# Performance work log

Measured on AMD Instinct MI355X. Metric: run time of the kernel, lower is better.

## Reference

```python
import jax, jax.numpy as jnp
import numpy as np

N_NODES, N_EDGES, MAX_NB = 40000, 80000, 4
INPUT_SIZE, NODE_FDIM, HIDDEN = 384, 256, 256
DEPTH = 6


def setup_inputs() -> dict:
    key = jax.random.key(0)
    ks = jax.random.split(key, 16)
    s = 0.05  # weight init scale
    return {
        "fnode": jax.random.normal(ks[0], (N_NODES, NODE_FDIM), dtype=jnp.float32),
        "fmess": jax.random.normal(ks[1], (N_EDGES, INPUT_SIZE), dtype=jnp.float32),
        "agraph": jax.random.randint(ks[2], (N_NODES, MAX_NB), 0, N_EDGES),
        "bgraph": jax.random.randint(ks[3], (N_EDGES, MAX_NB), 0, N_EDGES),
        "mask": jnp.ones((N_NODES, 1), dtype=jnp.float32),
        "Wz": jax.random.normal(ks[4], (INPUT_SIZE + HIDDEN, HIDDEN), dtype=jnp.float32) * s,
        "bz": jnp.zeros((HIDDEN,), dtype=jnp.float32),
        "Wr": jax.random.normal(ks[5], (INPUT_SIZE, HIDDEN), dtype=jnp.float32) * s,
        "Ur": jax.random.normal(ks[6], (HIDDEN, HIDDEN), dtype=jnp.float32) * s,
        "bur": jnp.zeros((HIDDEN,), dtype=jnp.float32),
        "Wh": jax.random.normal(ks[7], (INPUT_SIZE + HIDDEN, HIDDEN), dtype=jnp.float32) * s,
        "bh": jnp.zeros((HIDDEN,), dtype=jnp.float32),
        "Wo": jax.random.normal(ks[8], (NODE_FDIM + HIDDEN, HIDDEN), dtype=jnp.float32) * s,
        "bo": jnp.zeros((HIDDEN,), dtype=jnp.float32),
        "depth": DEPTH,
    }


def reference(fnode, fmess, agraph, bgraph, mask, Wz, bz, Wr, Ur, bur, Wh, bh, Wo, bo, depth):
    E, H = fmess.shape[0], Wz.shape[1]
    # message 0 is padding -> kept at zero each step (mask[0,0]=0 in torch GRU)
    msg_mask = jnp.ones((E, 1), dtype=fmess.dtype).at[0, 0].set(0.0)
    rx = fmess @ Wr  # precomputable: [E, H], reset gate input term

    def step(h, _):
        h_nei = h[bgraph]                      # [E, nb, H] gather
        sum_h = h_nei.sum(axis=1)              # [E, H]
        z = jax.nn.sigmoid(jnp.concatenate([fmess, sum_h], axis=1) @ Wz + bz)
        r = jax.nn.sigmoid(rx[:, None, :] + h_nei @ Ur + bur)  # [E, nb, H]
        sum_gh = (r * h_nei).sum(axis=1)
        pre_h = jnp.tanh(jnp.concatenate([fmess, sum_gh], axis=1) @ Wh + bh)
        h_new = ((1.0 - z) * sum_h + z * pre_h) * msg_mask
        return h_new, None

    h0 = jnp.zeros((E, H), dtype=fmess.dtype)
    h, _ = jax.lax.scan(step, h0, None, length=depth)

    nei_message = h[agraph].sum(axis=1)        # [N, H] gather-sum over incoming edges
    node_hiddens = jax.nn.relu(jnp.concatenate([fnode, nei_message], axis=1) @ Wo + bo)
    return node_hiddens * mask, h
```

## Files before the change

kernel.cpp:

```cpp
#include <hip/hip_runtime.h>
#include <stdint.h>

#define N_NODES 40000
#define N_EDGES 80000
#define HID 256
#define DEPTH_FIXED 6
#define NPAD 40064
#define MT 32

typedef __bf16 bf16;
typedef __bf16 bf16x4 __attribute__((ext_vector_type(4)));
typedef __bf16 bf16x8 __attribute__((ext_vector_type(8)));
typedef float f32x4 __attribute__((ext_vector_type(4)));

#define TPAD 136
#define APAD 264

__device__ __forceinline__ float sigmoidf_(float x) { return 1.f / (1.f + __expf(-x)); }
__device__ __forceinline__ float tanhf_(float x) { float e = __expf(2.f * x); return 1.f - 2.f / (e + 1.f); }

__device__ __forceinline__ void gld_lds16(const void* g, void* l) {
    __builtin_amdgcn_global_load_lds(
        (const __attribute__((address_space(1))) uint32_t*)g,
        (__attribute__((address_space(3))) uint32_t*)l, 16, 0, 0);
}

__device__ __forceinline__ void stage_tile(const bf16* __restrict__ src, int ld, int r0, int k0,
                                           bf16* lds, int tid) {
#pragma unroll
    for (int jj = 0; jj < 2; ++jj) {
        int s = jj * 256 + tid;
        int c = s ^ ((s >> 3) & 3);
        gld_lds16(src + (size_t)(r0 + (c >> 2)) * ld + k0 + (c & 3) * 8, lds + s * 8);
    }
}

__device__ __forceinline__ void mfma_tile(const bf16* lds_a, const bf16* lds_b,
                                          int wm, int wn, int lane, f32x4 (&acc)[4][4]) {
    const int li = lane & 15, quad = lane >> 4;
    const int sw = quad ^ ((li >> 1) & 3);
    bf16x8 a[4], b[4];
#pragma unroll
    for (int i = 0; i < 4; ++i)
        a[i] = *(const bf16x8*)(lds_a + ((wm * 64 + i * 16 + li) * 4 + sw) * 8);
#pragma unroll
    for (int j = 0; j < 4; ++j)
        b[j] = *(const bf16x8*)(lds_b + ((wn * 64 + j * 16 + li) * 4 + sw) * 8);
#pragma unroll
    for (int i = 0; i < 4; ++i)
#pragma unroll
        for (int j = 0; j < 4; ++j)
            acc[i][j] = __builtin_amdgcn_mfma_f32_16x16x32_bf16(a[i], b[j], acc[i][j], 0, 0, 0);
}

__global__ __launch_bounds__(256, 3) void step_fused_k(
    const int* __restrict__ bgraph, const bf16* __restrict__ Hcur,
    const bf16* __restrict__ HU, const bf16* __restrict__ P,
    const bf16* __restrict__ B1T, const bf16* __restrict__ B2T,
    bf16* __restrict__ Hnew, float* __restrict__ HF) {
    __shared__ __align__(16) bf16 sA1[MT * APAD];
    __shared__ __align__(16) bf16 sA2[MT * APAD];
    __shared__ __align__(16) bf16 sBst[256 * 32];
    const int tid = threadIdx.x, lane = tid & 63, wave = tid >> 6;
    const int m0 = blockIdx.x * MT;

    {
        const int r = tid >> 3, qc = tid & 7;
        const int e = m0 + r;
        const int4 nb = *(const int4*)(bgraph + (size_t)e * 4);
        const int bi[4] = {nb.x, nb.y, nb.z, nb.w};
        const bf16* prx = P + (size_t)e * 768 + qc * 32;
        bf16x8 rx[4];
#pragma unroll
        for (int c = 0; c < 4; ++c) rx[c] = *(const bf16x8*)(prx + c * 8);
        float sh[4][8] = {}, gh[4][8] = {};
#pragma unroll
        for (int j = 0; j < 4; ++j) {
            const bf16* hp = Hcur + (size_t)bi[j] * HID + qc * 32;
            const bf16* up = HU + (size_t)bi[j] * HID + qc * 32;
            bf16x8 hv[4], uv[4];
#pragma unroll
            for (int c = 0; c < 4; ++c) { hv[c] = *(const bf16x8*)(hp + c * 8); uv[c] = *(const bf16x8*)(up + c * 8); }
#pragma unroll
            for (int c = 0; c < 4; ++c)
#pragma unroll
                for (int u = 0; u < 8; ++u) {
                    float hf = (float)hv[c][u];
                    float rr = sigmoidf_((float)rx[c][u] + (float)uv[c][u]);
                    sh[c][u] += hf;
                    gh[c][u] += rr * hf;
                }
        }
#pragma unroll
        for (int c = 0; c < 4; ++c) {
            bf16x8 os, og;
#pragma unroll
            for (int u = 0; u < 8; ++u) { os[u] = (bf16)sh[c][u]; og[u] = (bf16)gh[c][u]; }
            *(bf16x8*)(sA1 + r * APAD + qc * 32 + c * 8) = os;
            *(bf16x8*)(sA2 + r * APAD + qc * 32 + c * 8) = og;
        }
    }
    __syncthreads();

    const int li = lane & 15, quad = lane >> 4;
    const int sw = quad ^ ((li >> 1) & 3);
    f32x4 accZ[2][4] = {}, accH[2][4] = {};
#pragma unroll
    for (int pass = 0; pass < 2; ++pass) {
        const bf16* BT = pass ? B2T : B1T;
        const bf16* sA = pass ? sA2 : sA1;
        for (int t = 0; t < 8; ++t) {
#pragma unroll
            for (int jj = 0; jj < 4; ++jj) {
                int s = jj * 256 + tid;
                int c = s ^ ((s >> 3) & 3);
                gld_lds16(BT + (size_t)(c >> 2) * 256 + t * 32 + (c & 3) * 8, sBst + s * 8);
            }
            __syncthreads();
            bf16x8 a[2], b[4];
#pragma unroll
            for (int i = 0; i < 2; ++i)
                a[i] = *(const bf16x8*)(sA + (i * 16 + li) * APAD + t * 32 + quad * 8);
#pragma unroll
            for (int j = 0; j < 4; ++j)
                b[j] = *(const bf16x8*)(sBst + ((wave * 64 + j * 16 + li) * 4 + sw) * 8);
#pragma unroll
            for (int i = 0; i < 2; ++i)
#pragma unroll
                for (int j = 0; j < 4; ++j) {
                    if (pass == 0) accZ[i][j] = __builtin_amdgcn_mfma_f32_16x16x32_bf16(a[i], b[j], accZ[i][j], 0, 0, 0);
                    else           accH[i][j] = __builtin_amdgcn_mfma_f32_16x16x32_bf16(a[i], b[j], accH[i][j], 0, 0, 0);
                }
            __syncthreads();
        }
    }

    bf16* tZ = sA2;
    bf16* tH = sBst;
#pragma unroll
    for (int i = 0; i < 2; ++i)
#pragma unroll
        for (int j = 0; j < 4; ++j) {
            const int col = wave * 64 + j * 16 + li;
#pragma unroll
            for (int r = 0; r < 4; ++r) {
                const int row = i * 16 + quad * 4 + r;
                tZ[row * APAD + col] = (bf16)accZ[i][j][r];
                tH[row * 256 + col] = (bf16)accH[i][j][r];
            }
        }
    __syncthreads();
#pragma unroll
    for (int s = 0; s < 4; ++s) {
        int v = s * 256 + tid;
        int lr = v >> 5, c8 = (v & 31) * 8;
        int e = m0 + lr;
        bf16x8 zl = *(const bf16x8*)(tZ + lr * APAD + c8);
        bf16x8 hl = *(const bf16x8*)(tH + lr * 256 + c8);
        bf16x8 shv = *(const bf16x8*)(sA1 + lr * APAD + c8);
        bf16x8 zx = *(const bf16x8*)(P + (size_t)e * 768 + 256 + c8);
        bf16x8 hx = *(const bf16x8*)(P + (size_t)e * 768 + 512 + c8);
        bf16x8 o;
        float of[8];
#pragma unroll
        for (int u = 0; u < 8; ++u) {
            float z = sigmoidf_((float)zl[u] + (float)zx[u]);
            float p = tanhf_((float)hl[u] + (float)hx[u]);
            float hn = (1.f - z) * (float)shv[u] + z * p;
            if (e == 0) hn = 0.f;
            o[u] = (bf16)hn;
            of[u] = hn;
        }
        *(bf16x8*)(Hnew + (size_t)e * HID + c8) = o;
        if (HF) {
            *(float4*)(HF + (size_t)e * HID + c8) = make_float4(of[0], of[1], of[2], of[3]);
            *(float4*)(HF + (size_t)e * HID + c8 + 4) = make_float4(of[4], of[5], of[6], of[7]);
        }
    }
}

__global__ __launch_bounds__(256) void gemm_single_k(
    const bf16* __restrict__ A, const bf16* __restrict__ BT,
    const float* __restrict__ bias, bf16* __restrict__ C, int K, int ldc) {
    __shared__ __align__(16) char smem[34816];
    bf16* sA = (bf16*)smem;
    bf16* sB = sA + 4096;
    const int tid = threadIdx.x, lane = tid & 63, wave = tid >> 6;
    const int wm = wave >> 1, wn = wave & 1;
    const int m0 = blockIdx.x * 128, n0 = blockIdx.y * 128;
    f32x4 acc[4][4] = {};
    for (int k0 = 0; k0 < K; k0 += 32) {
        stage_tile(A, K, m0, k0, sA, tid);
        stage_tile(BT, K, n0, k0, sB, tid);
        __syncthreads();
        mfma_tile(sA, sB, wm, wn, lane, acc);
        __syncthreads();
    }
    bf16* tC = (bf16*)smem;
#pragma unroll
    for (int i = 0; i < 4; ++i)
#pragma unroll
        for (int j = 0; j < 4; ++j) {
            const int col = wn * 64 + j * 16 + (lane & 15);
#pragma unroll
            for (int r = 0; r < 4; ++r) {
                const int lr = wm * 64 + i * 16 + (lane >> 4) * 4 + r;
                tC[lr * TPAD + col] = (bf16)acc[i][j][r];
            }
        }
    __syncthreads();
#pragma unroll
    for (int s = 0; s < 8; ++s) {
        int v = s * 256 + tid;
        int lr = v >> 4, c8 = (v & 15) * 8;
        bf16x8 cv = *(const bf16x8*)(tC + lr * TPAD + c8);
        bf16x8 o;
        if (bias) {
            float4 b0 = *(const float4*)(bias + n0 + c8);
            float4 b1 = *(const float4*)(bias + n0 + c8 + 4);
            o[0] = (bf16)((float)cv[0] + b0.x); o[1] = (bf16)((float)cv[1] + b0.y);
            o[2] = (bf16)((float)cv[2] + b0.z); o[3] = (bf16)((float)cv[3] + b0.w);
            o[4] = (bf16)((float)cv[4] + b1.x); o[5] = (bf16)((float)cv[5] + b1.y);
            o[6] = (bf16)((float)cv[6] + b1.z); o[7] = (bf16)((float)cv[7] + b1.w);
        } else {
            o = cv;
        }
        *(bf16x8*)(C + (size_t)(m0 + lr) * ldc + n0 + c8) = o;
    }
}

__global__ __launch_bounds__(256) void gemm_out_k(
    const bf16* __restrict__ A1, const bf16* __restrict__ A2,
    const bf16* __restrict__ B1T, const bf16* __restrict__ B2T,
    const float* __restrict__ bo, const float* __restrict__ mask, float* __restrict__ out) {
    __shared__ __align__(16) char smem[34816];
    bf16* s0 = (bf16*)smem;
    bf16* s1 = s0 + 4096;
    bf16* s2 = s1 + 4096;
    bf16* s3 = s2 + 4096;
    const int tid = threadIdx.x, lane = tid & 63, wave = tid >> 6;
    const int wm = wave >> 1, wn = wave & 1;
    const int m0 = blockIdx.x * 128, n0 = blockIdx.y * 128;
    f32x4 acc1[4][4] = {}, acc2[4][4] = {};
    for (int k0 = 0; k0 < 256; k0 += 32) {
        stage_tile(A1, 256, m0, k0, s0, tid);
        stage_tile(B1T, 256, n0, k0, s1, tid);
        stage_tile(A2, 256, m0, k0, s2, tid);
        stage_tile(B2T, 256, n0, k0, s3, tid);
        __syncthreads();
        mfma_tile(s0, s1, wm, wn, lane, acc1);
        mfma_tile(s2, s3, wm, wn, lane, acc2);
        __syncthreads();
    }
    bf16* tC = (bf16*)smem;
#pragma unroll
    for (int i = 0; i < 4; ++i)
#pragma unroll
        for (int j = 0; j < 4; ++j) {
            const int col = wn * 64 + j * 16 + (lane & 15);
#pragma unroll
            for (int r = 0; r < 4; ++r) {
                const int lr = wm * 64 + i * 16 + (lane >> 4) * 4 + r;
                tC[lr * TPAD + col] = (bf16)(acc1[i][j][r] + acc2[i][j][r]);
            }
        }
    __syncthreads();
#pragma unroll
    for (int s = 0; s < 8; ++s) {
        int v = s * 256 + tid;
        int lr = v >> 4, c8 = (v & 15) * 8;
        int grow = m0 + lr;
        if (grow >= N_NODES) continue;
        int gcol = n0 + c8;
        bf16x8 cv = *(const bf16x8*)(tC + lr * TPAD + c8);
        float4 b0 = *(const float4*)(bo + gcol);
        float4 b1 = *(const float4*)(bo + gcol + 4);
        float mk = mask[grow];
        float4 o0, o1;
        o0.x = fmaxf((float)cv[0] + b0.x, 0.f) * mk;
        o0.y = fmaxf((float)cv[1] + b0.y, 0.f) * mk;
        o0.z = fmaxf((float)cv[2] + b0.z, 0.f) * mk;
        o0.w = fmaxf((float)cv[3] + b0.w, 0.f) * mk;
        o1.x = fmaxf((float)cv[4] + b1.x, 0.f) * mk;
        o1.y = fmaxf((float)cv[5] + b1.y, 0.f) * mk;
        o1.z = fmaxf((float)cv[6] + b1.z, 0.f) * mk;
        o1.w = fmaxf((float)cv[7] + b1.w, 0.f) * mk;
        *(float4*)(out + (size_t)grow * 256 + gcol) = o0;
        *(float4*)(out + (size_t)grow * 256 + gcol + 4) = o1;
    }
}

__global__ __launch_bounds__(256) void gather_nei_k(
    const int* __restrict__ agraph, const bf16* __restrict__ H, bf16* __restrict__ nei) {
    int i = blockIdx.x * 256 + threadIdx.x;
    int v = i >> 5, c8 = (i & 31) * 8;
    bf16x8 o;
    if (v < N_NODES) {
        int4 nb = *(const int4*)(agraph + (size_t)v * 4);
        int bi[4] = {nb.x, nb.y, nb.z, nb.w};
        float s[8] = {};
#pragma unroll
        for (int j = 0; j < 4; ++j) {
            bf16x8 hv = *(const bf16x8*)(H + (size_t)bi[j] * HID + c8);
#pragma unroll
            for (int r = 0; r < 8; ++r) s[r] += (float)hv[r];
        }
#pragma unroll
        for (int r = 0; r < 8; ++r) o[r] = (bf16)s[r];
    } else {
#pragma unroll
        for (int r = 0; r < 8; ++r) o[r] = (bf16)0.f;
    }
    *(bf16x8*)(nei + (size_t)v * HID + c8) = o;
}

__global__ __launch_bounds__(256) void step1_k(const bf16* __restrict__ P, bf16* __restrict__ H) {
    int i = blockIdx.x * 256 + threadIdx.x;
    int e = i >> 5, c8 = (i & 31) * 8;
    bf16x8 zx = *(const bf16x8*)(P + (size_t)e * 768 + 256 + c8);
    bf16x8 hx = *(const bf16x8*)(P + (size_t)e * 768 + 512 + c8);
    bf16x8 o;
#pragma unroll
    for (int r = 0; r < 8; ++r) {
        float h = sigmoidf_((float)zx[r]) * tanhf_((float)hx[r]);
        if (e == 0) h = 0.f;
        o[r] = (bf16)h;
    }
    *(bf16x8*)(H + (size_t)e * HID + c8) = o;
}

__global__ void cvt_bf16_k(const float* __restrict__ src, bf16* __restrict__ dst, int n4) {
    int i = blockIdx.x * 256 + threadIdx.x;
    if (i >= n4) return;
    float4 v = ((const float4*)src)[i];
    bf16x4 o = {(bf16)v.x, (bf16)v.y, (bf16)v.z, (bf16)v.w};
    *((bf16x4*)dst + i) = o;
}

__global__ void cvt_fnode_k(const float* __restrict__ src, bf16* __restrict__ dst) {
    int i = blockIdx.x * 256 + threadIdx.x;
    int row = i >> 6;
    bf16x4 o = {(bf16)0.f, (bf16)0.f, (bf16)0.f, (bf16)0.f};
    if (row < N_NODES) {
        float4 v = ((const float4*)src)[i];
        o[0] = (bf16)v.x; o[1] = (bf16)v.y; o[2] = (bf16)v.z; o[3] = (bf16)v.w;
    }
    *((bf16x4*)dst + i) = o;
}

__global__ void prep_wpre_k(const float* __restrict__ Wr, const float* __restrict__ Wz,
                            const float* __restrict__ Wh, bf16* __restrict__ WT) {
    int idx = blockIdx.x * 256 + threadIdx.x;
    if (idx >= 768 * 384) return;
    int n = idx / 384, k = idx % 384;
    float v;
    if (n < 256) v = Wr[(size_t)k * 256 + n];
    else if (n < 512) v = Wz[(size_t)k * 256 + (n - 256)];
    else v = Wh[(size_t)k * 256 + (n - 512)];
    WT[idx] = (bf16)v;
}

__global__ void prep_bias_k(const float* __restrict__ bur, const float* __restrict__ bz,
                            const float* __restrict__ bh, float* __restrict__ bp) {
    int n = blockIdx.x * 256 + threadIdx.x;
    if (n >= 768) return;
    bp[n] = n < 256 ? bur[n] : (n < 512 ? bz[n - 256] : bh[n - 512]);
}

__global__ void prep_t256_k(const float* __restrict__ W, bf16* __restrict__ T, int roff) {
    int idx = blockIdx.x * 256 + threadIdx.x;
    int n = idx >> 8, k = idx & 255;
    T[idx] = (bf16)W[(size_t)(roff + k) * 256 + n];
}

extern "C" void kernel_launch(void* const* d_in, const int* in_sizes, int n_in,
                              void* d_out, int out_size, void* d_ws, size_t ws_size,
                              hipStream_t stream) {
    (void)in_sizes; (void)n_in; (void)out_size; (void)ws_size;
    const float* fnode = (const float*)d_in[0];
    const float* fmess = (const float*)d_in[1];
    const int* agraph = (const int*)d_in[2];
    const int* bgraph = (const int*)d_in[3];
    const float* mask = (const float*)d_in[4];
    const float* Wz = (const float*)d_in[5];
    const float* bz = (const float*)d_in[6];
    const float* Wr = (const float*)d_in[7];
    const float* Ur = (const float*)d_in[8];
    const float* bur = (const float*)d_in[9];
    const float* Wh = (const float*)d_in[10];
    const float* bh = (const float*)d_in[11];
    const float* Wo = (const float*)d_in[12];
    const float* bo = (const float*)d_in[13];
    float* out_node = (float*)d_out;
    float* out_h = out_node + (size_t)N_NODES * HID;

    char* ws = (char*)d_ws;
    size_t off = 0;
    auto alloc = [&](size_t b) -> char* { char* p = ws + off; off += (b + 255) & ~(size_t)255; return p; };
    bf16* P     = (bf16*)alloc((size_t)N_EDGES * 768 * 2);
    bf16* Hb0   = (bf16*)alloc((size_t)N_EDGES * HID * 2);
    bf16* Hb1   = (bf16*)alloc((size_t)N_EDGES * HID * 2);
    bf16* HU    = (bf16*)alloc((size_t)N_EDGES * HID * 2);
    bf16* fnodeB= (bf16*)alloc((size_t)NPAD * HID * 2);
    bf16* nei   = (bf16*)alloc((size_t)NPAD * HID * 2);
    bf16* WTpre = (bf16*)alloc((size_t)768 * 384 * 2);
    bf16* UrT   = (bf16*)alloc(65536 * 2);
    bf16* WzBT  = (bf16*)alloc(65536 * 2);
    bf16* WhBT  = (bf16*)alloc(65536 * 2);
    bf16* WoTT  = (bf16*)alloc(65536 * 2);
    bf16* WoBT  = (bf16*)alloc(65536 * 2);
    float* biasP= (float*)alloc(768 * 4);
    bf16* fmessB = Hb1;

    cvt_bf16_k<<<30000, 256, 0, stream>>>(fmess, fmessB, N_EDGES * 384 / 4);
    cvt_fnode_k<<<NPAD * 64 / 256, 256, 0, stream>>>(fnode, fnodeB);
    prep_wpre_k<<<(768 * 384 + 255) / 256, 256, 0, stream>>>(Wr, Wz, Wh, WTpre);
    prep_bias_k<<<3, 256, 0, stream>>>(bur, bz, bh, biasP);
    prep_t256_k<<<256, 256, 0, stream>>>(Ur, UrT, 0);
    prep_t256_k<<<256, 256, 0, stream>>>(Wz, WzBT, 384);
    prep_t256_k<<<256, 256, 0, stream>>>(Wh, WhBT, 384);
    prep_t256_k<<<256, 256, 0, stream>>>(Wo, WoTT, 0);
    prep_t256_k<<<256, 256, 0, stream>>>(Wo, WoBT, 256);

    gemm_single_k<<<dim3(625, 6), 256, 0, stream>>>(fmessB, WTpre, biasP, P, 384, 768);

    step1_k<<<N_EDGES * 32 / 256, 256, 0, stream>>>(P, Hb0);

    bf16* cur = Hb0;
    bf16* nxt = Hb1;
    for (int d = 2; d <= DEPTH_FIXED; ++d) {
        gemm_single_k<<<dim3(625, 2), 256, 0, stream>>>(cur, UrT, nullptr, HU, 256, 256);
        step_fused_k<<<N_EDGES / MT, 256, 0, stream>>>(bgraph, cur, HU, P, WzBT, WhBT, nxt,
                                                       d == DEPTH_FIXED ? out_h : nullptr);
        bf16* t = cur; cur = nxt; nxt = t;
    }

    gather_nei_k<<<NPAD * 32 / 256, 256, 0, stream>>>(agraph, cur, nei);
    gemm_out_k<<<dim3(313, 2), 256, 0, stream>>>(fnodeB, nei, WoTT, WoBT, bo, mask, out_node);
}
```

Measured before the change: 1.395 ms.

## Interleave H and H·Ur rows, read weights directly from global, drop staging LDS

H and its Ur projection now share one interleaved buffer with a 512-element row stride, so each neighbor gather reads a single contiguous 1 KB row instead of two separate rows. The fused step kernel no longer stages weight tiles into shared memory. Each wave loads its B fragments straight from global or L2, which removes per-tile barriers and the sBst buffer. The epilogue is split into two column halves so the transpose scratch fits in sA2, and the occupancy hint rises from 3 to 4 blocks. The risk is extra global and L2 traffic for the weights, since every block now rereads them without LDS reuse across waves.

```diff
diff --git a/kernel.cpp b/kernel.cpp
--- a/kernel.cpp
+++ b/kernel.cpp
@@ -15,6 +15,7 @@
 
 #define TPAD 136
 #define APAD 264
+#define TP2  132
 
 __device__ __forceinline__ float sigmoidf_(float x) { return 1.f / (1.f + __expf(-x)); }
 __device__ __forceinline__ float tanhf_(float x) { float e = __expf(2.f * x); return 1.f - 2.f / (e + 1.f); }
@@ -53,16 +54,16 @@
             acc[i][j] = __builtin_amdgcn_mfma_f32_16x16x32_bf16(a[i], b[j], acc[i][j], 0, 0, 0);
 }
 
-__global__ __launch_bounds__(256, 3) void step_fused_k(
-    const int* __restrict__ bgraph, const bf16* __restrict__ Hcur,
-    const bf16* __restrict__ HU, const bf16* __restrict__ P,
+__global__ __launch_bounds__(256, 4) void step_fused_k(
+    const int* __restrict__ bgraph, const bf16* __restrict__ HH,
+    const bf16* __restrict__ P,
     const bf16* __restrict__ B1T, const bf16* __restrict__ B2T,
-    bf16* __restrict__ Hnew, float* __restrict__ HF) {
+    bf16* __restrict__ HHn, float* __restrict__ HF) {
     __shared__ __align__(16) bf16 sA1[MT * APAD];
     __shared__ __align__(16) bf16 sA2[MT * APAD];
-    __shared__ __align__(16) bf16 sBst[256 * 32];
     const int tid = threadIdx.x, lane = tid & 63, wave = tid >> 6;
     const int m0 = blockIdx.x * MT;
+    const int li = lane & 15, quad = lane >> 4;
 
     {
         const int r = tid >> 3, qc = tid & 7;
@@ -76,11 +77,10 @@
         float sh[4][8] = {}, gh[4][8] = {};
 #pragma unroll
         for (int j = 0; j < 4; ++j) {
-            const bf16* hp = Hcur + (size_t)bi[j] * HID + qc * 32;
-            const bf16* up = HU + (size_t)bi[j] * HID + qc * 32;
+            const bf16* hp = HH + (size_t)bi[j] * 512 + qc * 32;
             bf16x8 hv[4], uv[4];
 #pragma unroll
-            for (int c = 0; c < 4; ++c) { hv[c] = *(const bf16x8*)(hp + c * 8); uv[c] = *(const bf16x8*)(up + c * 8); }
+            for (int c = 0; c < 4; ++c) { hv[c] = *(const bf16x8*)(hp + c * 8); uv[c] = *(const bf16x8*)(hp + 256 + c * 8); }
 #pragma unroll
             for (int c = 0; c < 4; ++c)
 #pragma unroll
@@ -102,85 +102,94 @@
     }
     __syncthreads();
 
-    const int li = lane & 15, quad = lane >> 4;
-    const int sw = quad ^ ((li >> 1) & 3);
     f32x4 accZ[2][4] = {}, accH[2][4] = {};
-#pragma unroll
-    for (int pass = 0; pass < 2; ++pass) {
-        const bf16* BT = pass ? B2T : B1T;
-        const bf16* sA = pass ? sA2 : sA1;
+    {
+        const bf16* bbase1 = B1T + (size_t)(wave * 64 + li) * 256 + quad * 8;
         for (int t = 0; t < 8; ++t) {
-#pragma unroll
-            for (int jj = 0; jj < 4; ++jj) {
-                int s = jj * 256 + tid;
-                int c = s ^ ((s >> 3) & 3);
-                gld_lds16(BT + (size_t)(c >> 2) * 256 + t * 32 + (c & 3) * 8, sBst + s * 8);
+            bf16x8 a[2], b[4];
+#pragma unroll
+            for (int i = 0; i < 2; ++i)
+                a[i] = *(const bf16x8*)(sA1 + (i * 16 + li) * APAD + t * 32 + quad * 8);
+#pragma unroll
+            for (int j = 0; j < 4; ++j)
+                b[j] = *(const bf16x8*)(bbase1 + j * 16 * 256 + t * 32);
+#pragma unroll
+            for (int i = 0; i < 2; ++i)
+#pragma unroll
+                for (int j = 0; j < 4; ++j)
+                    accZ[i][j] = __builtin_amdgcn_mfma_f32_16x16x32_bf16(a[i], b[j], accZ[i][j], 0, 0, 0);
+        }
+        const bf16* bbase2 = B2T + (size_t)(wave * 64 + li) * 256 + quad * 8;
+        for (int t = 0; t < 8; ++t) {
+            bf16x8 a[2], b[4];
+#pragma unroll
+            for (int i = 0; i < 2; ++i)
+                a[i] = *(const bf16x8*)(sA2 + (i * 16 + li) * APAD + t * 32 + quad * 8);
+#pragma unroll
+            for (int j = 0; j < 4; ++j)
+                b[j] = *(const bf16x8*)(bbase2 + j * 16 * 256 + t * 32);
+#pragma unroll
+            for (int i = 0; i < 2; ++i)
+#pragma unroll
+                for (int j = 0; j < 4; ++j)
+                    accH[i][j] = __builtin_amdgcn_mfma_f32_16x16x32_bf16(a[i], b[j], accH[i][j], 0, 0, 0);
+        }
+    }
+
+    bf16* tZh = sA2;
+    bf16* tHh = sA2 + MT * TP2;
+#pragma unroll
+    for (int half = 0; half < 2; ++half) {
+        __syncthreads();
+        if ((wave >> 1) == half) {
+            const int colbase = (wave & 1) * 64;
+#pragma unroll
+            for (int i = 0; i < 2; ++i)
+#pragma unroll
+                for (int j = 0; j < 4; ++j) {
+                    const int col = colbase + j * 16 + li;
+#pragma unroll
+                    for (int r = 0; r < 4; ++r) {
+                        const int row = i * 16 + quad * 4 + r;
+                        tZh[row * TP2 + col] = (bf16)accZ[i][j][r];
+                        tHh[row * TP2 + col] = (bf16)accH[i][j][r];
+                    }
+                }
+        }
+        __syncthreads();
+#pragma unroll
+        for (int s = 0; s < 2; ++s) {
+            int v = s * 256 + tid;
+            int lr = v >> 4, c = (v & 15) * 8;
+            int e = m0 + lr;
+            int gcol = half * 128 + c;
+            bf16x8 zl = *(const bf16x8*)(tZh + lr * TP2 + c);
+            bf16x8 hl = *(const bf16x8*)(tHh + lr * TP2 + c);
+            bf16x8 shv = *(const bf16x8*)(sA1 + lr * APAD + gcol);
+            bf16x8 zx = *(const bf16x8*)(P + (size_t)e * 768 + 256 + gcol);
+            bf16x8 hx = *(const bf16x8*)(P + (size_t)e * 768 + 512 + gcol);
+            bf16x8 o;
+            float of[8];
+#pragma unroll
+            for (int u = 0; u < 8; ++u) {
+                float z = sigmoidf_((float)zl[u] + (float)zx[u]);
+                float p = tanhf_((float)hl[u] + (float)hx[u]);
+                float hn = (1.f - z) * (float)shv[u] + z * p;
+                if (e == 0) hn = 0.f;
+                o[u] = (bf16)hn;
+                of[u] = hn;
             }
-            __syncthreads();
-            bf16x8 a[2], b[4];
-#pragma unroll
-            for (int i = 0; i < 2; ++i)
-                a[i] = *(const bf16x8*)(sA + (i * 16 + li) * APAD + t * 32 + quad * 8);
-#pragma unroll
-            for (int j = 0; j < 4; ++j)
-                b[j] = *(const bf16x8*)(sBst + ((wave * 64 + j * 16 + li) * 4 + sw) * 8);
-#pragma unroll
-            for (int i = 0; i < 2; ++i)
-#pragma unroll
-                for (int j = 0; j < 4; ++j) {
-                    if (pass == 0) accZ[i][j] = __builtin_amdgcn_mfma_f32_16x16x32_bf16(a[i], b[j], accZ[i][j], 0, 0, 0);
-                    else           accH[i][j] = __builtin_amdgcn_mfma_f32_16x16x32_bf16(a[i], b[j], accH[i][j], 0, 0, 0);
-                }
-            __syncthreads();
-        }
-    }
-
-    bf16* tZ = sA2;
-    bf16* tH = sBst;
-#pragma unroll
-    for (int i = 0; i < 2; ++i)
-#pragma unroll
-        for (int j = 0; j < 4; ++j) {
-            const int col = wave * 64 + j * 16 + li;
-#pragma unroll
-            for (int r = 0; r < 4; ++r) {
-                const int row = i * 16 + quad * 4 + r;
-                tZ[row * APAD + col] = (bf16)accZ[i][j][r];
-                tH[row * 256 + col] = (bf16)accH[i][j][r];
+            *(bf16x8*)(HHn + (size_t)e * 512 + gcol) = o;
+            if (HF) {
+                *(float4*)(HF + (size_t)e * HID + gcol) = make_float4(of[0], of[1], of[2], of[3]);
+                *(float4*)(HF + (size_t)e * HID + gcol + 4) = make_float4(of[4], of[5], of[6], of[7]);
             }
         }
-    __syncthreads();
-#pragma unroll
-    for (int s = 0; s < 4; ++s) {
-        int v = s * 256 + tid;
-        int lr = v >> 5, c8 = (v & 31) * 8;
-        int e = m0 + lr;
-        bf16x8 zl = *(const bf16x8*)(tZ + lr * APAD + c8);
-        bf16x8 hl = *(const bf16x8*)(tH + lr * 256 + c8);
-        bf16x8 shv = *(const bf16x8*)(sA1 + lr * APAD + c8);
-        bf16x8 zx = *(const bf16x8*)(P + (size_t)e * 768 + 256 + c8);
-        bf16x8 hx = *(const bf16x8*)(P + (size_t)e * 768 + 512 + c8);
-        bf16x8 o;
-        float of[8];
-#pragma unroll
-        for (int u = 0; u < 8; ++u) {
-            float z = sigmoidf_((float)zl[u] + (float)zx[u]);
-            float p = tanhf_((float)hl[u] + (float)hx[u]);
-            float hn = (1.f - z) * (float)shv[u] + z * p;
-            if (e == 0) hn = 0.f;
-            o[u] = (bf16)hn;
-            of[u] = hn;
-        }
-        *(bf16x8*)(Hnew + (size_t)e * HID + c8) = o;
-        if (HF) {
-            *(float4*)(HF + (size_t)e * HID + c8) = make_float4(of[0], of[1], of[2], of[3]);
-            *(float4*)(HF + (size_t)e * HID + c8 + 4) = make_float4(of[4], of[5], of[6], of[7]);
-        }
     }
 }
 
 __global__ __launch_bounds__(256) void gemm_single_k(
-    const bf16* __restrict__ A, const bf16* __restrict__ BT,
+    const bf16* __restrict__ A, int lda, const bf16* __restrict__ BT,
     const float* __restrict__ bias, bf16* __restrict__ C, int K, int ldc) {
     __shared__ __align__(16) char smem[34816];
     bf16* sA = (bf16*)smem;
@@ -190,7 +199,7 @@
     const int m0 = blockIdx.x * 128, n0 = blockIdx.y * 128;
     f32x4 acc[4][4] = {};
     for (int k0 = 0; k0 < K; k0 += 32) {
-        stage_tile(A, K, m0, k0, sA, tid);
+        stage_tile(A, lda, m0, k0, sA, tid);
         stage_tile(BT, K, n0, k0, sB, tid);
         __syncthreads();
         mfma_tile(sA, sB, wm, wn, lane, acc);
@@ -291,7 +300,7 @@
 }
 
 __global__ __launch_bounds__(256) void gather_nei_k(
-    const int* __restrict__ agraph, const bf16* __restrict__ H, bf16* __restrict__ nei) {
+    const int* __restrict__ agraph, const bf16* __restrict__ HH, bf16* __restrict__ nei) {
     int i = blockIdx.x * 256 + threadIdx.x;
     int v = i >> 5, c8 = (i & 31) * 8;
     bf16x8 o;
@@ -301,7 +310,7 @@
         float s[8] = {};
 #pragma unroll
         for (int j = 0; j < 4; ++j) {
-            bf16x8 hv = *(const bf16x8*)(H + (size_t)bi[j] * HID + c8);
+            bf16x8 hv = *(const bf16x8*)(HH + (size_t)bi[j] * 512 + c8);
 #pragma unroll
             for (int r = 0; r < 8; ++r) s[r] += (float)hv[r];
         }
@@ -314,7 +323,7 @@
     *(bf16x8*)(nei + (size_t)v * HID + c8) = o;
 }
 
-__global__ __launch_bounds__(256) void step1_k(const bf16* __restrict__ P, bf16* __restrict__ H) {
+__global__ __launch_bounds__(256) void step1_k(const bf16* __restrict__ P, bf16* __restrict__ HH) {
     int i = blockIdx.x * 256 + threadIdx.x;
     int e = i >> 5, c8 = (i & 31) * 8;
     bf16x8 zx = *(const bf16x8*)(P + (size_t)e * 768 + 256 + c8);
@@ -326,7 +335,7 @@
         if (e == 0) h = 0.f;
         o[r] = (bf16)h;
     }
-    *(bf16x8*)(H + (size_t)e * HID + c8) = o;
+    *(bf16x8*)(HH + (size_t)e * 512 + c8) = o;
 }
 
 __global__ void cvt_bf16_k(const float* __restrict__ src, bf16* __restrict__ dst, int n4) {
@@ -398,9 +407,8 @@
     size_t off = 0;
     auto alloc = [&](size_t b) -> char* { char* p = ws + off; off += (b + 255) & ~(size_t)255; return p; };
     bf16* P     = (bf16*)alloc((size_t)N_EDGES * 768 * 2);
-    bf16* Hb0   = (bf16*)alloc((size_t)N_EDGES * HID * 2);
-    bf16* Hb1   = (bf16*)alloc((size_t)N_EDGES * HID * 2);
-    bf16* HU    = (bf16*)alloc((size_t)N_EDGES * HID * 2);
+    bf16* HH0   = (bf16*)alloc((size_t)N_EDGES * 512 * 2);
+    bf16* HH1   = (bf16*)alloc((size_t)N_EDGES * 512 * 2);
     bf16* fnodeB= (bf16*)alloc((size_t)NPAD * HID * 2);
     bf16* nei   = (bf16*)alloc((size_t)NPAD * HID * 2);
     bf16* WTpre = (bf16*)alloc((size_t)768 * 384 * 2);
@@ -410,7 +418,7 @@
     bf16* WoTT  = (bf16*)alloc(65536 * 2);
     bf16* WoBT  = (bf16*)alloc(65536 * 2);
     float* biasP= (float*)alloc(768 * 4);
-    bf16* fmessB = Hb1;
+    bf16* fmessB = HH1;
 
     cvt_bf16_k<<<30000, 256, 0, stream>>>(fmess, fmessB, N_EDGES * 384 / 4);
     cvt_fnode_k<<<NPAD * 64 / 256, 256, 0, stream>>>(fnode, fnodeB);
@@ -422,15 +430,15 @@
     prep_t256_k<<<256, 256, 0, stream>>>(Wo, WoTT, 0);
     prep_t256_k<<<256, 256, 0, stream>>>(Wo, WoBT, 256);
 
-    gemm_single_k<<<dim3(625, 6), 256, 0, stream>>>(fmessB, WTpre, biasP, P, 384, 768);
-
-    step1_k<<<N_EDGES * 32 / 256, 256, 0, stream>>>(P, Hb0);
-
-    bf16* cur = Hb0;
-    bf16* nxt = Hb1;
+    gemm_single_k<<<dim3(625, 6), 256, 0, stream>>>(fmessB, 384, WTpre, biasP, P, 384, 768);
+
+    step1_k<<<N_EDGES * 32 / 256, 256, 0, stream>>>(P, HH0);
+
+    bf16* cur = HH0;
+    bf16* nxt = HH1;
     for (int d = 2; d <= DEPTH_FIXED; ++d) {
-        gemm_single_k<<<dim3(625, 2), 256, 0, stream>>>(cur, UrT, nullptr, HU, 256, 256);
-        step_fused_k<<<N_EDGES / MT, 256, 0, stream>>>(bgraph, cur, HU, P, WzBT, WhBT, nxt,
+        gemm_single_k<<<dim3(625, 2), 256, 0, stream>>>(cur, 512, UrT, nullptr, cur + 256, 256, 512);
+        step_fused_k<<<N_EDGES / MT, 256, 0, stream>>>(bgraph, cur, P, WzBT, WhBT, nxt,
                                                        d == DEPTH_FIXED ? out_h : nullptr);
         bf16* t = cur; cur = nxt; nxt = t;
     }
```

Result: slower. 1.747 ms (+25.3%).
